# Kernel optimization log

Measured on AMD Instinct MI355X. Metric: run time of the kernel, lower is better.

Reference implementation:

```python
import jax, jax.numpy as jnp
import numpy as np

BN_EPS = 1e-5

def setup_inputs() -> dict:
    key = jax.random.key(0)
    ks = jax.random.split(key, 6)
    N, D, H = 1024, 256, 128
    scale = 0.05
    return {
        "graph_embeddings": jax.random.normal(ks[0], (N, D), jnp.float32),
        "W1": jax.random.normal(ks[1], (2 * D, H), jnp.float32) * scale,
        "b1": jnp.zeros((H,), jnp.float32),
        "W2": jax.random.normal(ks[2], (H, 1), jnp.float32) * scale,
        "b2": jnp.zeros((1,), jnp.float32),
        "Wg": jax.random.normal(ks[3], (D, H), jnp.float32) * scale,
        "bg": jnp.zeros((H,), jnp.float32),
        "gamma": jnp.ones((H,), jnp.float32),
        "beta": jnp.zeros((H,), jnp.float32),
    }

def reference(graph_embeddings, W1, b1, W2, b2, Wg, bg, gamma, beta):
    N, D = graph_embeddings.shape
    # Pairwise similarity MLP: sim(i,j) = sigmoid(W2 @ relu(W1 @ [x_i; x_j] + b1) + b2)
    # Split W1 over the concat dim so we never materialize [N,N,2D].
    a = graph_embeddings @ W1[:D]          # [N, H] contribution of x_i
    c = graph_embeddings @ W1[D:]          # [N, H] contribution of x_j
    h = jax.nn.relu(a[:, None, :] + c[None, :, :] + b1)   # [N, N, H]
    sim = jax.nn.sigmoid(jnp.einsum('ijh,h->ij', h, W2[:, 0]) + b2[0])  # [N, N]
    # Torch loop uses sim(i,j) with i<j for both directions; keep edge iff sim > 0.5.
    U = jnp.triu(sim, k=1)
    A = jnp.where(U > 0.5, U, 0.0)
    A = A + A.T + jnp.eye(N, dtype=sim.dtype)  # symmetric + GCN self-loops (weight 1)
    # GCN symmetric normalization: D^{-1/2} A D^{-1/2}
    deg = A.sum(axis=1)
    dis = jax.lax.rsqrt(deg)
    A_hat = A * dis[:, None] * dis[None, :]
    out = A_hat @ (graph_embeddings @ Wg) + bg  # [N, H]
    # BatchNorm1d (training mode: batch stats, biased variance)
    mean = out.mean(axis=0)
    var = out.var(axis=0)
    out = gamma * (out - mean) * jax.lax.rsqrt(var + BN_EPS) + beta
    return jax.nn.relu(out)
```

## Files before the change

kernel.cpp:

```cpp
#include <hip/hip_runtime.h>
#include <math.h>

constexpr int NN = 1024;
constexpr int DD = 256;
constexpr int HH = 128;
constexpr float BN_EPS = 1e-5f;

constexpr int OFF_A      = 0;
constexpr int OFF_AP     = OFF_A + NN * NN;
constexpr int OFF_CP     = OFF_AP + NN * HH;
constexpr int OFF_Y      = OFF_CP + NN * HH;
constexpr int OFF_DEG    = OFF_Y + NN * HH;
constexpr int OFF_STATS  = OFF_DEG + NN;
constexpr int OFF_OUTPRE = OFF_STATS + 256;

__global__ __launch_bounds__(256) void k1_gemm(
    const float* __restrict__ X, const float* __restrict__ W1,
    const float* __restrict__ Wg, const float* __restrict__ b1,
    float* __restrict__ aP, float* __restrict__ cP, float* __restrict__ Y,
    float* __restrict__ deg, float* __restrict__ stats) {
  const int tid = threadIdx.x;
  const int blk = blockIdx.x;
  if (blk >= 192) {
    if (blk == 192) {
      for (int i = tid; i < NN; i += 256) deg[i] = 0.f;
    } else {
      stats[tid] = 0.f;
    }
    return;
  }
  __shared__ float xs[16 * 256];
  __shared__ float ws[64 * 128];
  const int i0 = (blk & 63) * 16;
  const int m = blk >> 6;
  const float* W = (m == 0) ? W1 : (m == 1 ? W1 + DD * HH : Wg);
  const float* Xbase = X + i0 * DD;
#pragma unroll
  for (int v = 0; v < 4; ++v) {
    const int fi = (v * 256 + tid) * 4;
    *(float4*)(xs + fi) = *(const float4*)(Xbase + fi);
  }
  const int tx = tid & 31, ty = tid >> 5;
  float4 acc0 = make_float4(0.f, 0.f, 0.f, 0.f);
  float4 acc1 = make_float4(0.f, 0.f, 0.f, 0.f);
  for (int c = 0; c < 4; ++c) {
    __syncthreads();
    const float* Wbase = W + c * 64 * HH;
#pragma unroll
    for (int v = 0; v < 8; ++v) {
      const int fi = (v * 256 + tid) * 4;
      *(float4*)(ws + fi) = *(const float4*)(Wbase + fi);
    }
    __syncthreads();
    const float* xr0 = xs + (ty * 2) * 256 + c * 64;
    const float* xr1 = xs + (ty * 2 + 1) * 256 + c * 64;
#pragma unroll 4
    for (int d = 0; d < 64; d += 4) {
      const float4 x0 = *(const float4*)(xr0 + d);
      const float4 x1 = *(const float4*)(xr1 + d);
      const float4 w0 = *(const float4*)(ws + (d + 0) * 128 + tx * 4);
      const float4 w1 = *(const float4*)(ws + (d + 1) * 128 + tx * 4);
      const float4 w2 = *(const float4*)(ws + (d + 2) * 128 + tx * 4);
      const float4 w3 = *(const float4*)(ws + (d + 3) * 128 + tx * 4);
      acc0.x = fmaf(x0.x, w0.x, acc0.x); acc0.y = fmaf(x0.x, w0.y, acc0.y);
      acc0.z = fmaf(x0.x, w0.z, acc0.z); acc0.w = fmaf(x0.x, w0.w, acc0.w);
      acc1.x = fmaf(x1.x, w0.x, acc1.x); acc1.y = fmaf(x1.x, w0.y, acc1.y);
      acc1.z = fmaf(x1.x, w0.z, acc1.z); acc1.w = fmaf(x1.x, w0.w, acc1.w);
      acc0.x = fmaf(x0.y, w1.x, acc0.x); acc0.y = fmaf(x0.y, w1.y, acc0.y);
      acc0.z = fmaf(x0.y, w1.z, acc0.z); acc0.w = fmaf(x0.y, w1.w, acc0.w);
      acc1.x = fmaf(x1.y, w1.x, acc1.x); acc1.y = fmaf(x1.y, w1.y, acc1.y);
      acc1.z = fmaf(x1.y, w1.z, acc1.z); acc1.w = fmaf(x1.y, w1.w, acc1.w);
      acc0.x = fmaf(x0.z, w2.x, acc0.x); acc0.y = fmaf(x0.z, w2.y, acc0.y);
      acc0.z = fmaf(x0.z, w2.z, acc0.z); acc0.w = fmaf(x0.z, w2.w, acc0.w);
      acc1.x = fmaf(x1.z, w2.x, acc1.x); acc1.y = fmaf(x1.z, w2.y, acc1.y);
      acc1.z = fmaf(x1.z, w2.z, acc1.z); acc1.w = fmaf(x1.z, w2.w, acc1.w);
      acc0.x = fmaf(x0.w, w3.x, acc0.x); acc0.y = fmaf(x0.w, w3.y, acc0.y);
      acc0.z = fmaf(x0.w, w3.z, acc0.z); acc0.w = fmaf(x0.w, w3.w, acc0.w);
      acc1.x = fmaf(x1.w, w3.x, acc1.x); acc1.y = fmaf(x1.w, w3.y, acc1.y);
      acc1.z = fmaf(x1.w, w3.z, acc1.z); acc1.w = fmaf(x1.w, w3.w, acc1.w);
    }
  }
  float* dst = (m == 0) ? aP : (m == 1 ? cP : Y);
  if (m == 0) {
    const float4 bv = *(const float4*)(b1 + tx * 4);
    acc0.x += bv.x; acc0.y += bv.y; acc0.z += bv.z; acc0.w += bv.w;
    acc1.x += bv.x; acc1.y += bv.y; acc1.z += bv.z; acc1.w += bv.w;
  }
  const int r0 = i0 + ty * 2;
  *(float4*)(dst + r0 * HH + tx * 4) = acc0;
  *(float4*)(dst + (r0 + 1) * HH + tx * 4) = acc1;
}

__global__ __launch_bounds__(256) void k2_pairwise(
    const float* __restrict__ aP, const float* __restrict__ cP,
    const float* __restrict__ W2, const float* __restrict__ b2,
    float* __restrict__ A, float* __restrict__ deg) {
  __shared__ float as[32 * 132];
  __shared__ float cs[32 * 132];
  __shared__ float es[32 * 33];
  __shared__ float ws2[128];
  const int tid = threadIdx.x;
  int tt = blockIdx.x, ti = 0;
  while (tt >= 32 - ti) { tt -= 32 - ti; ++ti; }
  const int tj = ti + tt;
  const int i0 = ti * 32, j0 = tj * 32;
  if (tid < 32) *(float4*)(ws2 + tid * 4) = *(const float4*)(W2 + tid * 4);
  for (int idx = tid; idx < 32 * HH; idx += 256) {
    const int row = idx >> 7, col = idx & 127;
    as[row * 132 + col] = aP[(i0 + row) * HH + col];
    cs[row * 132 + col] = cP[(j0 + row) * HH + col];
  }
  __syncthreads();
  const int li0 = (tid >> 4) * 2, lj0 = (tid & 15) * 2;
  float s00 = 0.f, s01 = 0.f, s10 = 0.f, s11 = 0.f;
#pragma unroll 8
  for (int h = 0; h < HH; h += 4) {
    const float4 a0 = *(const float4*)(as + li0 * 132 + h);
    const float4 a1 = *(const float4*)(as + (li0 + 1) * 132 + h);
    const float4 c0 = *(const float4*)(cs + lj0 * 132 + h);
    const float4 c1 = *(const float4*)(cs + (lj0 + 1) * 132 + h);
    const float4 w = *(const float4*)(ws2 + h);
    s00 += fmaxf(a0.x + c0.x, 0.f) * w.x + fmaxf(a0.y + c0.y, 0.f) * w.y +
           fmaxf(a0.z + c0.z, 0.f) * w.z + fmaxf(a0.w + c0.w, 0.f) * w.w;
    s01 += fmaxf(a0.x + c1.x, 0.f) * w.x + fmaxf(a0.y + c1.y, 0.f) * w.y +
           fmaxf(a0.z + c1.z, 0.f) * w.z + fmaxf(a0.w + c1.w, 0.f) * w.w;
    s10 += fmaxf(a1.x + c0.x, 0.f) * w.x + fmaxf(a1.y + c0.y, 0.f) * w.y +
           fmaxf(a1.z + c0.z, 0.f) * w.z + fmaxf(a1.w + c0.w, 0.f) * w.w;
    s11 += fmaxf(a1.x + c1.x, 0.f) * w.x + fmaxf(a1.y + c1.y, 0.f) * w.y +
           fmaxf(a1.z + c1.z, 0.f) * w.z + fmaxf(a1.w + c1.w, 0.f) * w.w;
  }
  const float b2v = b2[0];
  auto edge = [b2v](float s) {
    s += b2v;
    return s > 0.f ? 1.f / (1.f + __expf(-s)) : 0.f;
  };
  es[(li0 + 0) * 33 + lj0 + 0] = edge(s00);
  es[(li0 + 0) * 33 + lj0 + 1] = edge(s01);
  es[(li0 + 1) * 33 + lj0 + 0] = edge(s10);
  es[(li0 + 1) * 33 + lj0 + 1] = edge(s11);
  __syncthreads();
  if (ti == tj) {
    float f[2][2];
#pragma unroll
    for (int r = 0; r < 2; ++r)
#pragma unroll
      for (int c = 0; c < 2; ++c) {
        const int li = li0 + r, lj = lj0 + c;
        f[r][c] =
            (li == lj) ? 1.f : (li < lj ? es[li * 33 + lj] : es[lj * 33 + li]);
      }
    __syncthreads();
    es[(li0 + 0) * 33 + lj0 + 0] = f[0][0];
    es[(li0 + 0) * 33 + lj0 + 1] = f[0][1];
    es[(li0 + 1) * 33 + lj0 + 0] = f[1][0];
    es[(li0 + 1) * 33 + lj0 + 1] = f[1][1];
    __syncthreads();
  }
  if (tid < 32) {
    float s = 0.f;
#pragma unroll
    for (int c = 0; c < 32; ++c) s += es[tid * 33 + c];
    atomicAdd(deg + i0 + tid, s);
  } else if (tid < 64 && ti != tj) {
    const int c = tid - 32;
    float s = 0.f;
#pragma unroll
    for (int r = 0; r < 32; ++r) s += es[r * 33 + c];
    atomicAdd(deg + j0 + c, s);
  }
#pragma unroll
  for (int r = 0; r < 2; ++r)
#pragma unroll
    for (int c = 0; c < 2; ++c) {
      const int li = li0 + r, lj = lj0 + c;
      A[(i0 + li) * NN + j0 + lj] = es[li * 33 + lj];
      if (ti != tj) A[(j0 + li) * NN + i0 + lj] = es[lj * 33 + li];
    }
}

__global__ __launch_bounds__(256) void k3_spmm(
    const float* __restrict__ A, const float* __restrict__ Y,
    const float* __restrict__ deg, const float* __restrict__ bg,
    float* __restrict__ out_pre, float* __restrict__ stats) {
  __shared__ float Ast[NN * 4];
  __shared__ float disl[NN];
  __shared__ float red[8 * 520];
  __shared__ float sm1[256], sm2[256];
  const int tid = threadIdx.x;
  const int i0 = blockIdx.x * 4;
  {
    const float4 dv = *(const float4*)(deg + tid * 4);
    float4 r;
    r.x = rsqrtf(dv.x); r.y = rsqrtf(dv.y);
    r.z = rsqrtf(dv.z); r.w = rsqrtf(dv.w);
    *(float4*)(disl + tid * 4) = r;
  }
  __syncthreads();
  const float* Ab = A + i0 * NN;
#pragma unroll
  for (int v = 0; v < 4; ++v) {
    const int fi = (v * 256 + tid) * 4;
    const float4 av = *(const float4*)(Ab + fi);
    const int r = fi >> 10, j = fi & 1023;
    Ast[(j + 0) * 4 + r] = av.x * disl[j + 0];
    Ast[(j + 1) * 4 + r] = av.y * disl[j + 1];
    Ast[(j + 2) * 4 + r] = av.z * disl[j + 2];
    Ast[(j + 3) * 4 + r] = av.w * disl[j + 3];
  }
  __syncthreads();
  const int tx = tid & 31, ty = tid >> 5;
  const int jbase = ty * 128;
  float4 acc[4];
#pragma unroll
  for (int r = 0; r < 4; ++r) acc[r] = make_float4(0.f, 0.f, 0.f, 0.f);
  const float* Yb = Y + jbase * HH + tx * 4;
#pragma unroll 4
  for (int jj = 0; jj < 128; ++jj) {
    const float4 yv = *(const float4*)(Yb + jj * HH);
    const float4 ab = *(const float4*)(Ast + (jbase + jj) * 4);
    acc[0].x = fmaf(ab.x, yv.x, acc[0].x); acc[0].y = fmaf(ab.x, yv.y, acc[0].y);
    acc[0].z = fmaf(ab.x, yv.z, acc[0].z); acc[0].w = fmaf(ab.x, yv.w, acc[0].w);
    acc[1].x = fmaf(ab.y, yv.x, acc[1].x); acc[1].y = fmaf(ab.y, yv.y, acc[1].y);
    acc[1].z = fmaf(ab.y, yv.z, acc[1].z); acc[1].w = fmaf(ab.y, yv.w, acc[1].w);
    acc[2].x = fmaf(ab.z, yv.x, acc[2].x); acc[2].y = fmaf(ab.z, yv.y, acc[2].y);
    acc[2].z = fmaf(ab.z, yv.z, acc[2].z); acc[2].w = fmaf(ab.z, yv.w, acc[2].w);
    acc[3].x = fmaf(ab.w, yv.x, acc[3].x); acc[3].y = fmaf(ab.w, yv.y, acc[3].y);
    acc[3].z = fmaf(ab.w, yv.z, acc[3].z); acc[3].w = fmaf(ab.w, yv.w, acc[3].w);
  }
#pragma unroll
  for (int r = 0; r < 4; ++r)
    *(float4*)(red + ty * 520 + r * 128 + tx * 4) = acc[r];
  __syncthreads();
  const int h = tid & 127, rr = tid >> 7;
  float v0 = 0.f, v1 = 0.f;
#pragma unroll
  for (int t = 0; t < 8; ++t) {
    v0 += red[t * 520 + rr * 128 + h];
    v1 += red[t * 520 + (rr + 2) * 128 + h];
  }
  const float bgv = bg[h];
  v0 = v0 * disl[i0 + rr] + bgv;
  v1 = v1 * disl[i0 + rr + 2] + bgv;
  out_pre[(i0 + rr) * HH + h] = v0;
  out_pre[(i0 + rr + 2) * HH + h] = v1;
  sm1[rr * 128 + h] = v0 + v1;
  sm2[rr * 128 + h] = v0 * v0 + v1 * v1;
  __syncthreads();
  if (rr == 0) {
    atomicAdd(&stats[h], sm1[h] + sm1[128 + h]);
    atomicAdd(&stats[128 + h], sm2[h] + sm2[128 + h]);
  }
}

__global__ __launch_bounds__(256) void k4_bn(
    const float* __restrict__ out_pre, const float* __restrict__ stats,
    const float* __restrict__ gamma, const float* __restrict__ beta,
    float* __restrict__ out) {
  const int idx = blockIdx.x * 256 + threadIdx.x;
  const int h = idx & 127;
  const float mean = stats[h] * (1.f / NN);
  const float var = stats[128 + h] * (1.f / NN) - mean * mean;
  float v = (out_pre[idx] - mean) * rsqrtf(var + BN_EPS);
  v = gamma[h] * v + beta[h];
  out[idx] = fmaxf(v, 0.f);
}

extern "C" void kernel_launch(void* const* d_in, const int* in_sizes, int n_in,
                              void* d_out, int out_size, void* d_ws,
                              size_t ws_size, hipStream_t stream) {
  const float* X = (const float*)d_in[0];
  const float* W1 = (const float*)d_in[1];
  const float* b1 = (const float*)d_in[2];
  const float* W2 = (const float*)d_in[3];
  const float* b2 = (const float*)d_in[4];
  const float* Wg = (const float*)d_in[5];
  const float* bg = (const float*)d_in[6];
  const float* gamma = (const float*)d_in[7];
  const float* beta = (const float*)d_in[8];
  float* out = (float*)d_out;

  float* w = (float*)d_ws;
  float* A = w + OFF_A;
  float* aP = w + OFF_AP;
  float* cP = w + OFF_CP;
  float* Y = w + OFF_Y;
  float* deg = w + OFF_DEG;
  float* stats = w + OFF_STATS;
  float* out_pre = w + OFF_OUTPRE;

  k1_gemm<<<dim3(194), 256, 0, stream>>>(X, W1, Wg, b1, aP, cP, Y, deg, stats);
  k2_pairwise<<<dim3(528), 256, 0, stream>>>(aP, cP, W2, b2, A, deg);
  k3_spmm<<<dim3(256), 256, 0, stream>>>(A, Y, deg, bg, out_pre, stats);
  k4_bn<<<dim3(512), 256, 0, stream>>>(out_pre, stats, gamma, beta, out);
}
```

Baseline: 117.5 us.

## Split SpMM columns into halves with 8-row tiles and per-column BN reduction

The SpMM kernel now gives each block 8 rows and half of the j range, so each Y row loaded is reused across 8 output rows instead of 4. Partial results go to two transposed buffers (P0/P1), which the BN kernel sums before computing mean and variance per feature column with a block reduction. This removes the global atomics for BN statistics and the stats buffer zeroing. The cost is an extra partial buffer round trip, and the BN kernel now writes its output with a strided, uncoalesced pattern.

Result: faster. 110.9 us (-5.5%).

```diff
diff --git a/kernel.cpp b/kernel.cpp
--- a/kernel.cpp
+++ b/kernel.cpp
@@ -11,22 +11,18 @@
 constexpr int OFF_CP     = OFF_AP + NN * HH;
 constexpr int OFF_Y      = OFF_CP + NN * HH;
 constexpr int OFF_DEG    = OFF_Y + NN * HH;
-constexpr int OFF_STATS  = OFF_DEG + NN;
-constexpr int OFF_OUTPRE = OFF_STATS + 256;
+constexpr int OFF_P0     = OFF_DEG + NN;
+constexpr int OFF_P1     = OFF_P0 + NN * HH;
 
 __global__ __launch_bounds__(256) void k1_gemm(
     const float* __restrict__ X, const float* __restrict__ W1,
     const float* __restrict__ Wg, const float* __restrict__ b1,
     float* __restrict__ aP, float* __restrict__ cP, float* __restrict__ Y,
-    float* __restrict__ deg, float* __restrict__ stats) {
+    float* __restrict__ deg) {
   const int tid = threadIdx.x;
   const int blk = blockIdx.x;
   if (blk >= 192) {
-    if (blk == 192) {
-      for (int i = tid; i < NN; i += 256) deg[i] = 0.f;
-    } else {
-      stats[tid] = 0.f;
-    }
+    for (int i = tid; i < NN; i += 256) deg[i] = 0.f;
     return;
   }
   __shared__ float xs[16 * 256];
@@ -180,14 +176,15 @@
 
 __global__ __launch_bounds__(256) void k3_spmm(
     const float* __restrict__ A, const float* __restrict__ Y,
-    const float* __restrict__ deg, const float* __restrict__ bg,
-    float* __restrict__ out_pre, float* __restrict__ stats) {
-  __shared__ float Ast[NN * 4];
+    const float* __restrict__ deg, float* __restrict__ P0,
+    float* __restrict__ P1) {
+  __shared__ float Ast[512 * 12];
   __shared__ float disl[NN];
-  __shared__ float red[8 * 520];
-  __shared__ float sm1[256], sm2[256];
+  __shared__ float red[8 * 1032];
   const int tid = threadIdx.x;
-  const int i0 = blockIdx.x * 4;
+  const int rb = blockIdx.x >> 1, half = blockIdx.x & 1;
+  const int i0 = rb * 8, jh0 = half * 512;
+  float* __restrict__ P = half ? P1 : P0;
   {
     const float4 dv = *(const float4*)(deg + tid * 4);
     float4 r;
@@ -196,73 +193,88 @@
     *(float4*)(disl + tid * 4) = r;
   }
   __syncthreads();
-  const float* Ab = A + i0 * NN;
-#pragma unroll
-  for (int v = 0; v < 4; ++v) {
-    const int fi = (v * 256 + tid) * 4;
-    const float4 av = *(const float4*)(Ab + fi);
-    const int r = fi >> 10, j = fi & 1023;
-    Ast[(j + 0) * 4 + r] = av.x * disl[j + 0];
-    Ast[(j + 1) * 4 + r] = av.y * disl[j + 1];
-    Ast[(j + 2) * 4 + r] = av.z * disl[j + 2];
-    Ast[(j + 3) * 4 + r] = av.w * disl[j + 3];
+#pragma unroll
+  for (int v = 0; v < 2; ++v) {
+    const int jj = v * 256 + tid;
+    const int jg = jh0 + jj;
+    const float d = disl[jg];
+    float a[8];
+#pragma unroll
+    for (int r = 0; r < 8; ++r) a[r] = A[(i0 + r) * NN + jg] * d;
+    *(float4*)(Ast + jj * 12)     = make_float4(a[0], a[1], a[2], a[3]);
+    *(float4*)(Ast + jj * 12 + 4) = make_float4(a[4], a[5], a[6], a[7]);
   }
   __syncthreads();
   const int tx = tid & 31, ty = tid >> 5;
-  const int jbase = ty * 128;
-  float4 acc[4];
-#pragma unroll
-  for (int r = 0; r < 4; ++r) acc[r] = make_float4(0.f, 0.f, 0.f, 0.f);
-  const float* Yb = Y + jbase * HH + tx * 4;
+  const int jj0 = ty * 64;
+  float4 acc[8];
+#pragma unroll
+  for (int r = 0; r < 8; ++r) acc[r] = make_float4(0.f, 0.f, 0.f, 0.f);
+  const float* Yb = Y + (jh0 + jj0) * HH + tx * 4;
+#define FMA4(AC, S) \
+  AC.x = fmaf(S, yv.x, AC.x); AC.y = fmaf(S, yv.y, AC.y); \
+  AC.z = fmaf(S, yv.z, AC.z); AC.w = fmaf(S, yv.w, AC.w);
 #pragma unroll 4
-  for (int jj = 0; jj < 128; ++jj) {
+  for (int jj = 0; jj < 64; ++jj) {
     const float4 yv = *(const float4*)(Yb + jj * HH);
-    const float4 ab = *(const float4*)(Ast + (jbase + jj) * 4);
-    acc[0].x = fmaf(ab.x, yv.x, acc[0].x); acc[0].y = fmaf(ab.x, yv.y, acc[0].y);
-    acc[0].z = fmaf(ab.x, yv.z, acc[0].z); acc[0].w = fmaf(ab.x, yv.w, acc[0].w);
-    acc[1].x = fmaf(ab.y, yv.x, acc[1].x); acc[1].y = fmaf(ab.y, yv.y, acc[1].y);
-    acc[1].z = fmaf(ab.y, yv.z, acc[1].z); acc[1].w = fmaf(ab.y, yv.w, acc[1].w);
-    acc[2].x = fmaf(ab.z, yv.x, acc[2].x); acc[2].y = fmaf(ab.z, yv.y, acc[2].y);
-    acc[2].z = fmaf(ab.z, yv.z, acc[2].z); acc[2].w = fmaf(ab.z, yv.w, acc[2].w);
-    acc[3].x = fmaf(ab.w, yv.x, acc[3].x); acc[3].y = fmaf(ab.w, yv.y, acc[3].y);
-    acc[3].z = fmaf(ab.w, yv.z, acc[3].z); acc[3].w = fmaf(ab.w, yv.w, acc[3].w);
-  }
-#pragma unroll
-  for (int r = 0; r < 4; ++r)
-    *(float4*)(red + ty * 520 + r * 128 + tx * 4) = acc[r];
-  __syncthreads();
-  const int h = tid & 127, rr = tid >> 7;
-  float v0 = 0.f, v1 = 0.f;
-#pragma unroll
-  for (int t = 0; t < 8; ++t) {
-    v0 += red[t * 520 + rr * 128 + h];
-    v1 += red[t * 520 + (rr + 2) * 128 + h];
-  }
+    const float4 lo = *(const float4*)(Ast + (jj0 + jj) * 12);
+    const float4 hi = *(const float4*)(Ast + (jj0 + jj) * 12 + 4);
+    FMA4(acc[0], lo.x) FMA4(acc[1], lo.y) FMA4(acc[2], lo.z) FMA4(acc[3], lo.w)
+    FMA4(acc[4], hi.x) FMA4(acc[5], hi.y) FMA4(acc[6], hi.z) FMA4(acc[7], hi.w)
+  }
+#undef FMA4
+#pragma unroll
+  for (int r = 0; r < 8; ++r)
+    *(float4*)(red + ty * 1032 + r * 128 + tx * 4) = acc[r];
+  __syncthreads();
+  const int h = tid & 127, rg = tid >> 7;
+  float* Pcol = P + h * NN + i0;
+#pragma unroll
+  for (int k = 0; k < 4; ++k) {
+    const int row = rg + 2 * k;
+    float v = 0.f;
+#pragma unroll
+    for (int t = 0; t < 8; ++t) v += red[t * 1032 + row * 128 + h];
+    Pcol[row] = v * disl[i0 + row];
+  }
+}
+
+__global__ __launch_bounds__(256) void k4_bn(
+    const float* __restrict__ P0, const float* __restrict__ P1,
+    const float* __restrict__ bg, const float* __restrict__ gamma,
+    const float* __restrict__ beta, float* __restrict__ out) {
+  const int tid = threadIdx.x, h = blockIdx.x;
   const float bgv = bg[h];
-  v0 = v0 * disl[i0 + rr] + bgv;
-  v1 = v1 * disl[i0 + rr + 2] + bgv;
-  out_pre[(i0 + rr) * HH + h] = v0;
-  out_pre[(i0 + rr + 2) * HH + h] = v1;
-  sm1[rr * 128 + h] = v0 + v1;
-  sm2[rr * 128 + h] = v0 * v0 + v1 * v1;
-  __syncthreads();
-  if (rr == 0) {
-    atomicAdd(&stats[h], sm1[h] + sm1[128 + h]);
-    atomicAdd(&stats[128 + h], sm2[h] + sm2[128 + h]);
-  }
-}
-
-__global__ __launch_bounds__(256) void k4_bn(
-    const float* __restrict__ out_pre, const float* __restrict__ stats,
-    const float* __restrict__ gamma, const float* __restrict__ beta,
-    float* __restrict__ out) {
-  const int idx = blockIdx.x * 256 + threadIdx.x;
-  const int h = idx & 127;
-  const float mean = stats[h] * (1.f / NN);
-  const float var = stats[128 + h] * (1.f / NN) - mean * mean;
-  float v = (out_pre[idx] - mean) * rsqrtf(var + BN_EPS);
-  v = gamma[h] * v + beta[h];
-  out[idx] = fmaxf(v, 0.f);
+  const float4 p0 = *(const float4*)(P0 + h * NN + tid * 4);
+  const float4 p1 = *(const float4*)(P1 + h * NN + tid * 4);
+  float v[4] = {p0.x + p1.x + bgv, p0.y + p1.y + bgv,
+                p0.z + p1.z + bgv, p0.w + p1.w + bgv};
+  float s1 = v[0] + v[1] + v[2] + v[3];
+  float s2 = v[0] * v[0] + v[1] * v[1] + v[2] * v[2] + v[3] * v[3];
+  __shared__ float rs1[4], rs2[4], msh[2];
+#pragma unroll
+  for (int off = 32; off; off >>= 1) {
+    s1 += __shfl_down(s1, off);
+    s2 += __shfl_down(s2, off);
+  }
+  if ((tid & 63) == 0) { rs1[tid >> 6] = s1; rs2[tid >> 6] = s2; }
+  __syncthreads();
+  if (tid == 0) {
+    const float t1 = rs1[0] + rs1[1] + rs1[2] + rs1[3];
+    const float t2 = rs2[0] + rs2[1] + rs2[2] + rs2[3];
+    const float mean = t1 * (1.f / NN);
+    const float var = t2 * (1.f / NN) - mean * mean;
+    msh[0] = mean;
+    msh[1] = rsqrtf(var + BN_EPS);
+  }
+  __syncthreads();
+  const float mean = msh[0], rinv = msh[1];
+  const float g = gamma[h], be = beta[h];
+#pragma unroll
+  for (int k = 0; k < 4; ++k) {
+    const float val = g * (v[k] - mean) * rinv + be;
+    out[(tid * 4 + k) * HH + h] = fmaxf(val, 0.f);
+  }
 }
 
 extern "C" void kernel_launch(void* const* d_in, const int* in_sizes, int n_in,
@@ -285,11 +297,11 @@
   float* cP = w + OFF_CP;
   float* Y = w + OFF_Y;
   float* deg = w + OFF_DEG;
-  float* stats = w + OFF_STATS;
-  float* out_pre = w + OFF_OUTPRE;
-
-  k1_gemm<<<dim3(194), 256, 0, stream>>>(X, W1, Wg, b1, aP, cP, Y, deg, stats);
+  float* P0 = w + OFF_P0;
+  float* P1 = w + OFF_P1;
+
+  k1_gemm<<<dim3(193), 256, 0, stream>>>(X, W1, Wg, b1, aP, cP, Y, deg);
   k2_pairwise<<<dim3(528), 256, 0, stream>>>(aP, cP, W2, b2, A, deg);
-  k3_spmm<<<dim3(256), 256, 0, stream>>>(A, Y, deg, bg, out_pre, stats);
-  k4_bn<<<dim3(512), 256, 0, stream>>>(out_pre, stats, gamma, beta, out);
-}
+  k3_spmm<<<dim3(256), 256, 0, stream>>>(A, Y, deg, P0, P1);
+  k4_bn<<<dim3(128), 256, 0, stream>>>(P0, P1, bg, gamma, beta, out);
+}
```
